# Kernel tuning notes

Measured on AMD Instinct MI355X. Metric: run time of the kernel, lower is better.

The kernel has to match this reference:

```python
import jax, jax.numpy as jnp
import numpy as np

N_NODES = 10000
N_EDGES = 100000
IN_CH = 384
PROJ = 768  # in_channels * projection_factor
N_BLOCKS = 4
OUT_CH = 128
LN_EPS = 1e-5


def _p(key, shape, fan_in):
    return jax.random.normal(key, shape, dtype=jnp.float32) * (1.0 / np.sqrt(fan_in))


def setup_inputs() -> dict:
    key = jax.random.key(0)
    ks = iter(jax.random.split(key, 64))
    x = jax.random.normal(next(ks), (N_NODES, IN_CH), dtype=jnp.float32)
    edge_index = jax.random.randint(next(ks), (2, N_EDGES), 0, N_NODES, dtype=jnp.int64)
    inp = {
        'x': x,
        'edge_index': edge_index,
        'proj_W': _p(next(ks), (PROJ, IN_CH), IN_CH),
        'proj_b': jnp.zeros((PROJ,), jnp.float32),
        'norm_w': jnp.ones((N_BLOCKS, PROJ), jnp.float32),
        'norm_b': jnp.zeros((N_BLOCKS, PROJ), jnp.float32),
        'g1_W': _p(next(ks), (N_BLOCKS, 4 * 192, PROJ), PROJ),
        'g1_as': _p(next(ks), (N_BLOCKS, 4, 192), 192),
        'g1_ad': _p(next(ks), (N_BLOCKS, 4, 192), 192),
        'g1_b': jnp.zeros((N_BLOCKS, 4 * 192), jnp.float32),
        'g2_W': _p(next(ks), (N_BLOCKS, 2 * 96, PROJ), PROJ),
        'g2_as': _p(next(ks), (N_BLOCKS, 2, 96), 96),
        'g2_ad': _p(next(ks), (N_BLOCKS, 2, 96), 96),
        'g2_b': jnp.zeros((N_BLOCKS, 2 * 96), jnp.float32),
        'uni_W': _p(next(ks), (N_BLOCKS, PROJ, 960), 960),
        'uni_b': jnp.zeros((N_BLOCKS, PROJ), jnp.float32),
        'fnorm_w': jnp.ones((PROJ,), jnp.float32),
        'fnorm_b': jnp.zeros((PROJ,), jnp.float32),
        'fg_W': _p(next(ks), (8 * OUT_CH, PROJ), PROJ),
        'fg_as': _p(next(ks), (8, OUT_CH), OUT_CH),
        'fg_ad': _p(next(ks), (8, OUT_CH), OUT_CH),
        'fg_b': jnp.zeros((OUT_CH,), jnp.float32),
    }
    return inp


def layer_norm(x, w, b):
    m = x.mean(-1, keepdims=True)
    v = ((x - m) ** 2).mean(-1, keepdims=True)
    return (x - m) / jnp.sqrt(v + LN_EPS) * w + b


def gat_conv(x, src, dst, W, a_src, a_dst, bias, heads, out_ch, concat):
    # PyG GATConv (eval mode, add_self_loops already applied in src/dst).
    n = x.shape[0]
    h = (x @ W.T).reshape(n, heads, out_ch)          # [N,H,C]
    al_s = jnp.einsum('nhc,hc->nh', h, a_src)        # [N,H]
    al_d = jnp.einsum('nhc,hc->nh', h, a_dst)
    e = jax.nn.leaky_relu(al_s[src] + al_d[dst], 0.2)  # [E,H]
    emax = jax.ops.segment_max(e, dst, num_segments=n)
    ee = jnp.exp(e - emax[dst])
    den = jax.ops.segment_sum(ee, dst, num_segments=n)
    alpha = ee / (den[dst] + 1e-16)                  # softmax over incoming edges
    out = jax.ops.segment_sum(h[src] * alpha[:, :, None], dst, num_segments=n)
    out = out.reshape(n, heads * out_ch) if concat else out.mean(axis=1)
    return out + bias


def reference(x, edge_index, proj_W, proj_b, norm_w, norm_b,
              g1_W, g1_as, g1_ad, g1_b, g2_W, g2_as, g2_ad, g2_b,
              uni_W, uni_b, fnorm_w, fnorm_b, fg_W, fg_as, fg_ad, fg_b):
    n = x.shape[0]
    loop = jnp.arange(n, dtype=edge_index.dtype)
    src = jnp.concatenate([edge_index[0], loop])  # add self loops (PyG default)
    dst = jnp.concatenate([edge_index[1], loop])

    h = jax.nn.elu(x @ proj_W.T + proj_b)
    for i in range(N_BLOCKS):
        res = h
        hn = layer_norm(h, norm_w[i], norm_b[i])
        o1 = gat_conv(hn, src, dst, g1_W[i], g1_as[i], g1_ad[i], g1_b[i], 4, 192, True)
        o2 = gat_conv(hn, src, dst, g2_W[i], g2_as[i], g2_ad[i], g2_b[i], 2, 96, True)
        cat = jax.nn.elu(jnp.concatenate([o1, o2], axis=-1))  # [N,960]
        h = jax.nn.elu(res + cat @ uni_W[i].T + uni_b[i])
    h = layer_norm(h, fnorm_w, fnorm_b)
    return gat_conv(h, src, dst, fg_W, fg_as, fg_ad, fg_b, 8, OUT_CH, False)
```

## Files before the change

### kernel.cpp

```cpp
#include <hip/hip_runtime.h>
#include <math.h>

#define N_NODES 10000
#define N_EDGES 100000
#define E_TOT   (N_EDGES + N_NODES)
#define PROJ    768
#define LN_EPS  1e-5f

typedef __attribute__((ext_vector_type(8))) short bf16x8;
typedef __attribute__((ext_vector_type(4))) short bf16x4;
typedef __attribute__((ext_vector_type(4))) float f32x4;

__device__ __forceinline__ float elu_f(float x){ return x > 0.f ? x : __expf(x) - 1.f; }
__device__ __forceinline__ float bf2f(unsigned short u){ return __uint_as_float(((unsigned int)u) << 16); }
__device__ __forceinline__ unsigned short f2bf(float f){
  unsigned int u = __float_as_uint(f);
  return (unsigned short)((u + 0x7FFFu + ((u >> 16) & 1u)) >> 16);
}

#define GLOAD16(gp, lp) __builtin_amdgcn_global_load_lds((const __attribute__((address_space(1))) void*)(gp), (__attribute__((address_space(3))) void*)(lp), 16, 0, 0)

__global__ void k_count(const int* __restrict__ ei, int* __restrict__ cnt){
  int e = blockIdx.x*blockDim.x + threadIdx.x;
  if (e >= E_TOT) return;
  int dst = (e < N_EDGES) ? ei[N_EDGES + e] : (e - N_EDGES);
  atomicAdd(&cnt[dst], 1);
}

__global__ void k_scan(const int* __restrict__ cnt, int* __restrict__ indptr){
  __shared__ int s[1024];
  __shared__ int s_running;
  int t = threadIdx.x;
  if (t == 0) s_running = 0;
  __syncthreads();
  for (int base = 0; base < N_NODES; base += 1024){
    int v = (base + t < N_NODES) ? cnt[base + t] : 0;
    s[t] = v; __syncthreads();
    for (int off = 1; off < 1024; off <<= 1){
      int add = (t >= off) ? s[t - off] : 0;
      __syncthreads();
      s[t] += add;
      __syncthreads();
    }
    int total = s[1023];
    int run = s_running;
    if (base + t < N_NODES) indptr[base + t] = run + s[t] - v;
    __syncthreads();
    if (t == 0) s_running = run + total;
    __syncthreads();
  }
  if (t == 0) indptr[N_NODES] = s_running;
}

__global__ void k_copy_int(const int* __restrict__ src, int* __restrict__ dst, int n){
  int i = blockIdx.x*blockDim.x + threadIdx.x;
  if (i < n) dst[i] = src[i];
}

__global__ void k_fill(const int* __restrict__ ei, int* __restrict__ pos, int* __restrict__ csr_src){
  int e = blockIdx.x*blockDim.x + threadIdx.x;
  if (e >= E_TOT) return;
  int s, d;
  if (e < N_EDGES){ s = ei[e]; d = ei[N_EDGES + e]; }
  else            { s = d = e - N_EDGES; }
  int p = atomicAdd(&pos[d], 1);
  csr_src[p] = s;
}

__global__ void k_f2bf_arr4(const float4* __restrict__ in, ushort4* __restrict__ out, int n4){
  int i = blockIdx.x*blockDim.x + threadIdx.x;
  if (i < n4){
    float4 v = in[i];
    ushort4 o;
    o.x = f2bf(v.x); o.y = f2bf(v.y); o.z = f2bf(v.z); o.w = f2bf(v.w);
    out[i] = o;
  }
}

__global__ void k_pack_l1l2(const float* __restrict__ g1, const float* __restrict__ g2,
                            unsigned short* __restrict__ dst){
  int i = blockIdx.x*blockDim.x + threadIdx.x;
  if (i >= 737280) return;
  int layer = i / 184320;
  int off4  = i - layer*184320;
  float4 v;
  if (off4 < 147456) v = *((const float4*)(g1 + (size_t)layer*589824) + off4);
  else               v = *((const float4*)(g2 + (size_t)layer*147456) + (off4 - 147456));
  ushort4 o;
  o.x = f2bf(v.x); o.y = f2bf(v.y); o.z = f2bf(v.z); o.w = f2bf(v.w);
  ((ushort4*)(dst + (size_t)layer*737280))[off4] = o;
}

__global__ void k_layernorm_bf(const float* __restrict__ x, const float* __restrict__ w,
                               const float* __restrict__ b, unsigned short* __restrict__ y){
  int n = blockIdx.x;
  int t = threadIdx.x;
  const float* xr = x + (size_t)n*PROJ;
  float v0 = xr[t], v1 = xr[t+256], v2 = xr[t+512];
  float s  = v0+v1+v2;
  float s2 = v0*v0 + v1*v1 + v2*v2;
  #pragma unroll
  for (int off = 32; off; off >>= 1){ s += __shfl_down(s, off); s2 += __shfl_down(s2, off); }
  __shared__ float rs[4], rs2[4];
  __shared__ float s_mean, s_rstd;
  int wid = t >> 6, lane = t & 63;
  if (lane == 0){ rs[wid] = s; rs2[wid] = s2; }
  __syncthreads();
  if (t == 0){
    float S  = rs[0]+rs[1]+rs[2]+rs[3];
    float S2 = rs2[0]+rs2[1]+rs2[2]+rs2[3];
    float m  = S * (1.f/768.f);
    float var = S2 * (1.f/768.f) - m*m;
    s_mean = m; s_rstd = rsqrtf(var + LN_EPS);
  }
  __syncthreads();
  float m = s_mean, r = s_rstd;
  unsigned short* yr = y + (size_t)n*PROJ;
  yr[t]     = f2bf((v0-m)*r*w[t]     + b[t]);
  yr[t+256] = f2bf((v1-m)*r*w[t+256] + b[t+256]);
  yr[t+512] = f2bf((v2-m)*r*w[t+512] + b[t+512]);
}

template<int EPI>
__global__ __launch_bounds__(256)
void k_gemm_mfma(const unsigned short* __restrict__ A, int lda,
                 const unsigned short* __restrict__ W,
                 void* __restrict__ Cv, int ldc,
                 int M, int N, int K,
                 const float* __restrict__ bias,
                 const float* __restrict__ res, int ldres){
  __shared__ unsigned short As[128*32];
  __shared__ unsigned short Bs[128*32];
  const int bm = blockIdx.y*128, bn = blockIdx.x*128;
  const int tid = threadIdx.x;
  const int lane = tid & 63, wid = tid >> 6;
  const int wm = wid >> 1, wn = wid & 1;

  const int rowA0 = tid >> 2;
  const int c8 = (tid & 3) << 3;

  f32x4 acc[4][4];
  #pragma unroll
  for (int i=0;i<4;i++)
    #pragma unroll
    for (int j=0;j<4;j++) acc[i][j] = (f32x4){0.f,0.f,0.f,0.f};

  const size_t amr0 = (size_t)min(bm + rowA0,      M-1) * lda;
  const size_t amr1 = (size_t)min(bm + rowA0 + 64, M-1) * lda;
  const size_t wnr0 = (size_t)min(bn + rowA0,      N-1) * K;
  const size_t wnr1 = (size_t)min(bn + rowA0 + 64, N-1) * K;

  unsigned short* ldsA0 = &As[(wid*64)*8];
  unsigned short* ldsA1 = &As[(256 + wid*64)*8];
  unsigned short* ldsB0 = &Bs[(wid*64)*8];
  unsigned short* ldsB1 = &Bs[(256 + wid*64)*8];

  for (int k0 = 0; k0 < K; k0 += 32){
    __syncthreads();
    GLOAD16(A + amr0 + k0 + c8, ldsA0);
    GLOAD16(A + amr1 + k0 + c8, ldsA1);
    GLOAD16(W + wnr0 + k0 + c8, ldsB0);
    GLOAD16(W + wnr1 + k0 + c8, ldsB1);
    __syncthreads();

    bf16x8 af[4], bfr[4];
    const int kb8 = (lane >> 4) * 8;
    #pragma unroll
    for (int mi=0; mi<4; mi++){
      int r = wm*64 + mi*16 + (lane & 15);
      af[mi] = *(const bf16x8*)&As[r*32 + kb8];
    }
    #pragma unroll
    for (int ni=0; ni<4; ni++){
      int r = wn*64 + ni*16 + (lane & 15);
      bfr[ni] = *(const bf16x8*)&Bs[r*32 + kb8];
    }
    #pragma unroll
    for (int mi=0; mi<4; mi++)
      #pragma unroll
      for (int ni=0; ni<4; ni++)
        acc[mi][ni] = __builtin_amdgcn_mfma_f32_16x16x32_bf16(af[mi], bfr[ni], acc[mi][ni], 0,0,0);
  }

  const int mrow0 = bm + wm*64 + ((lane>>4)<<2);
  const int ncol0 = bn + wn*64 + (lane & 15);
  #pragma unroll
  for (int mi=0; mi<4; mi++){
    #pragma unroll
    for (int r=0; r<4; r++){
      int m = mrow0 + mi*16 + r;
      if (m >= M) continue;
      #pragma unroll
      for (int ni=0; ni<4; ni++){
        int n = ncol0 + ni*16;
        if (n >= N) continue;
        float v = acc[mi][ni][r];
        if (EPI == 0){
          ((unsigned short*)Cv)[(size_t)m*ldc + n] = f2bf(v);
        } else if (EPI == 1){
          ((float*)Cv)[(size_t)m*ldc + n] = elu_f(v + bias[n]);
        } else {
          ((float*)Cv)[(size_t)m*ldc + n] = elu_f(v + bias[n] + res[(size_t)m*ldres + n]);
        }
      }
    }
  }
}

template<int H, int C>
__global__ void k_attn_coef(const unsigned short* __restrict__ hlin, int ldh,
                            const float* __restrict__ a_src,
                            const float* __restrict__ a_dst,
                            float* __restrict__ als, float* __restrict__ ald){
  constexpr int CH = C/4;
  int n = blockIdx.x;
  int wid = threadIdx.x >> 6, lane = threadIdx.x & 63;
  float ss = 0.f, sd = 0.f;
  if (lane < CH){
    bf16x4 hv = *(const bf16x4*)(hlin + (size_t)n*ldh + wid*C + lane*4);
    float4 as_ = *(const float4*)&a_src[wid*C + lane*4];
    float4 ad_ = *(const float4*)&a_dst[wid*C + lane*4];
    float h0 = bf2f((unsigned short)hv.x), h1 = bf2f((unsigned short)hv.y);
    float h2 = bf2f((unsigned short)hv.z), h3 = bf2f((unsigned short)hv.w);
    ss = h0*as_.x + h1*as_.y + h2*as_.z + h3*as_.w;
    sd = h0*ad_.x + h1*ad_.y + h2*ad_.z + h3*ad_.w;
  }
  #pragma unroll
  for (int off = 32; off; off >>= 1){ ss += __shfl_down(ss, off); sd += __shfl_down(sd, off); }
  if (lane == 0){ als[n*H + wid] = ss; ald[n*H + wid] = sd; }
}

template<int H, int C, bool CONCAT, bool DO_ELU>
__global__ __launch_bounds__(256)
void k_attn_agg(const unsigned short* __restrict__ hlin, int ldh,
                const float* __restrict__ als, const float* __restrict__ ald,
                const int* __restrict__ indptr, const int* __restrict__ csr_src,
                const float* __restrict__ bias,
                void* __restrict__ outv, int ldo, int col0){
  constexpr int TOT = H*C;
  constexpr int CHUNKS = TOT/4;
  constexpr int CPL = (CHUNKS + 63)/64;
  int n = blockIdx.x;
  int tid = threadIdx.x;
  int wv = tid >> 6, lane = tid & 63;
  int beg = indptr[n], end = indptr[n+1];

  __shared__ float s_m[H], s_dinv[H], s_ald[H];
  __shared__ float s_red[4][TOT];

  for (int h = wv; h < H; h += 4){
    float aldv = ald[n*H + h];
    float m = -1e30f, d = 0.f;
    for (int e = beg + lane; e < end; e += 64){
      int s = csr_src[e];
      float v = als[s*H + h] + aldv;
      v = v > 0.f ? v : 0.2f*v;
      if (v > m){ d *= __expf(m - v); m = v; }
      d += __expf(v - m);
    }
    #pragma unroll
    for (int off = 1; off < 64; off <<= 1){
      float mo = __shfl_xor(m, off);
      float dd = __shfl_xor(d, off);
      float mn = fmaxf(m, mo);
      d = d*__expf(m - mn) + dd*__expf(mo - mn);
      m = mn;
    }
    if (lane == 0){ s_m[h] = m; s_dinv[h] = 1.f/(d + 1e-16f); s_ald[h] = aldv; }
  }
  __syncthreads();

  int hof[CPL];
  #pragma unroll
  for (int p = 0; p < CPL; p++) hof[p] = ((lane + p*64)*4)/C;

  f32x4 acc[CPL];
  #pragma unroll
  for (int p = 0; p < CPL; p++) acc[p] = (f32x4){0.f,0.f,0.f,0.f};

  for (int e = beg + wv; e < end; e += 4){
    int s = csr_src[e];
    float al = 0.f;
    if (lane < H){
      float v = als[s*H + lane] + s_ald[lane];
      v = v > 0.f ? v : 0.2f*v;
      al = __expf(v - s_m[lane]) * s_dinv[lane];
    }
    float aph[CPL];
    #pragma unroll
    for (int p = 0; p < CPL; p++) aph[p] = __shfl(al, hof[p]);
    const bf16x4* hr = (const bf16x4*)(hlin + (size_t)s*ldh);
    #pragma unroll
    for (int p = 0; p < CPL; p++){
      int ch = lane + p*64;
      if (CHUNKS % 64 == 0 || ch < CHUNKS){
        bf16x4 hv = hr[ch];
        acc[p].x += bf2f((unsigned short)hv.x)*aph[p];
        acc[p].y += bf2f((unsigned short)hv.y)*aph[p];
        acc[p].z += bf2f((unsigned short)hv.z)*aph[p];
        acc[p].w += bf2f((unsigned short)hv.w)*aph[p];
      }
    }
  }

  #pragma unroll
  for (int p = 0; p < CPL; p++){
    int ch = lane + p*64;
    if (CHUNKS % 64 == 0 || ch < CHUNKS)
      *(f32x4*)&s_red[wv][ch*4] = acc[p];
  }
  __syncthreads();

  if (CONCAT){
    unsigned short* out = (unsigned short*)outv;
    constexpr int QS = (TOT + 255)/256;
    #pragma unroll
    for (int q = 0; q < QS; q++){
      int idx = tid + q*256;
      if (TOT % 256 == 0 || idx < TOT){
        float v = s_red[0][idx] + s_red[1][idx] + s_red[2][idx] + s_red[3][idx] + bias[idx];
        if (DO_ELU) v = elu_f(v);
        out[(size_t)n*ldo + col0 + idx] = f2bf(v);
      }
    }
  } else {
    float* out = (float*)outv;
    if (tid < C){
      float v = 0.f;
      #pragma unroll
      for (int h = 0; h < H; h++){
        int idx = h*C + tid;
        v += s_red[0][idx] + s_red[1][idx] + s_red[2][idx] + s_red[3][idx];
      }
      out[(size_t)n*ldo + tid] = v*(1.f/(float)H) + bias[tid];
    }
  }
}

extern "C" void kernel_launch(void* const* d_in, const int* in_sizes, int n_in,
                              void* d_out, int out_size, void* d_ws, size_t ws_size,
                              hipStream_t stream){
  const float* x      = (const float*)d_in[0];
  const int*   ei     = (const int*)  d_in[1];
  const float* proj_W = (const float*)d_in[2];
  const float* proj_b = (const float*)d_in[3];
  const float* norm_w = (const float*)d_in[4];
  const float* norm_b = (const float*)d_in[5];
  const float* g1_W   = (const float*)d_in[6];
  const float* g1_as  = (const float*)d_in[7];
  const float* g1_ad  = (const float*)d_in[8];
  const float* g1_b   = (const float*)d_in[9];
  const float* g2_W   = (const float*)d_in[10];
  const float* g2_as  = (const float*)d_in[11];
  const float* g2_ad  = (const float*)d_in[12];
  const float* g2_b   = (const float*)d_in[13];
  const float* uni_W  = (const float*)d_in[14];
  const float* uni_b  = (const float*)d_in[15];
  const float* fnorm_w= (const float*)d_in[16];
  const float* fnorm_b= (const float*)d_in[17];
  const float* fg_W   = (const float*)d_in[18];
  const float* fg_as  = (const float*)d_in[19];
  const float* fg_ad  = (const float*)d_in[20];
  const float* fg_b   = (const float*)d_in[21];

  float* w = (float*)d_ws;
  float* h    = w; w += 7680000;
  float* h2   = w; w += 7680000;
  unsigned short* linbuf = (unsigned short*)w; w += 5120000;
  unsigned short* hnb  = (unsigned short*)w; w += 3840000;
  unsigned short* catb = (unsigned short*)w; w += 4800000;
  unsigned short* wb   = (unsigned short*)w; w += 3489792;
  float* als  = w; w += 80000;
  float* ald  = w; w += 80000;
  float* als2 = w; w += 80000;
  float* ald2 = w; w += 80000;
  int* iw = (int*)w;
  int* cnt     = iw; iw += 10016;
  int* indptr  = iw; iw += 10016;
  int* pos     = iw; iw += 10016;
  int* csr_src = iw; iw += 110016;

  unsigned short* wb_proj = wb;
  unsigned short* wb_l12  = wb_proj + 294912;
  unsigned short* wb_uni  = wb_l12 + 2949120;
  unsigned short* wb_fg   = wb_uni + 2949120;

  hipMemsetAsync(cnt, 0, N_NODES*sizeof(int), stream);
  k_count<<<(E_TOT+255)/256, 256, 0, stream>>>(ei, cnt);
  k_scan<<<1, 1024, 0, stream>>>(cnt, indptr);
  k_copy_int<<<(N_NODES+255)/256, 256, 0, stream>>>(indptr, pos, N_NODES);
  k_fill<<<(E_TOT+255)/256, 256, 0, stream>>>(ei, pos, csr_src);

  k_f2bf_arr4<<<(960000+255)/256, 256, 0, stream>>>((const float4*)x, (ushort4*)hnb, 960000);
  k_f2bf_arr4<<<(73728+255)/256,  256, 0, stream>>>((const float4*)proj_W, (ushort4*)wb_proj, 73728);
  k_pack_l1l2<<<(737280+255)/256, 256, 0, stream>>>(g1_W, g2_W, wb_l12);
  k_f2bf_arr4<<<(737280+255)/256, 256, 0, stream>>>((const float4*)uni_W, (ushort4*)wb_uni, 737280);
  k_f2bf_arr4<<<(196608+255)/256, 256, 0, stream>>>((const float4*)fg_W, (ushort4*)wb_fg, 196608);

  dim3 blk(256);
  const int GY = (N_NODES + 127) / 128;

  k_gemm_mfma<1><<<dim3(6, GY), blk, 0, stream>>>(hnb, 384, wb_proj, h, 768, N_NODES, 768, 384, proj_b, nullptr, 0);

  float* cur = h;
  float* oth = h2;
  for (int i = 0; i < 4; i++){
    k_layernorm_bf<<<N_NODES, 256, 0, stream>>>(cur, norm_w + i*768, norm_b + i*768, hnb);
    k_gemm_mfma<0><<<dim3(8, GY), blk, 0, stream>>>(hnb, 768, wb_l12 + (size_t)i*737280, linbuf, 960, N_NODES, 960, 768, nullptr, nullptr, 0);
    k_attn_coef<4,192><<<N_NODES, 256, 0, stream>>>(linbuf, 960, g1_as + i*768, g1_ad + i*768, als, ald);
    k_attn_agg<4,192,true,true><<<N_NODES, 256, 0, stream>>>(linbuf, 960, als, ald, indptr, csr_src, g1_b + i*768, catb, 960, 0);
    k_attn_coef<2,96><<<N_NODES, 128, 0, stream>>>(linbuf + 768, 960, g2_as + i*192, g2_ad + i*192, als2, ald2);
    k_attn_agg<2,96,true,true><<<N_NODES, 256, 0, stream>>>(linbuf + 768, 960, als2, ald2, indptr, csr_src, g2_b + i*192, catb, 960, 768);
    k_gemm_mfma<2><<<dim3(6, GY), blk, 0, stream>>>(catb, 960, wb_uni + (size_t)i*737280, oth, 768, N_NODES, 768, 960, uni_b + i*768, cur, 768);
    float* t = cur; cur = oth; oth = t;
  }

  k_layernorm_bf<<<N_NODES, 256, 0, stream>>>(cur, fnorm_w, fnorm_b, hnb);
  k_gemm_mfma<0><<<dim3(8, GY), blk, 0, stream>>>(hnb, 768, wb_fg, linbuf, 1024, N_NODES, 1024, 768, nullptr, nullptr, 0);
  k_attn_coef<8,128><<<N_NODES, 512, 0, stream>>>(linbuf, 1024, fg_as, fg_ad, als, ald);
  k_attn_agg<8,128,false,false><<<N_NODES, 256, 0, stream>>>(linbuf, 1024, als, ald, indptr, csr_src, fg_b, d_out, 128, 0);
}
```

Measured before the change: 835.9 us.

## Double-buffer GEMM LDS tiles with BK=64, XOR swizzle, and XCD-aware block mapping

The MFMA GEMM now loads K-tiles of 64 into two LDS buffers, prefetching the next tile with global_load_lds while computing on the current one. This removes the second barrier per iteration. LDS columns are XOR-swizzled to avoid bank conflicts, and the launch is flattened to a 1D grid remapped so consecutive tiles land on the same XCD for L2 reuse. Launch bounds now request 2 waves per SIMD. The cost is 64KB of LDS per block, which limits occupancy, and the kernel assumes K is a multiple of 64 (384, 768 and 960 all are).

New measurement: 789.6 us. -5.5%, faster.

```diff
diff --git a/kernel.cpp b/kernel.cpp
--- a/kernel.cpp
+++ b/kernel.cpp
@@ -122,22 +122,35 @@
 }
 
 template<int EPI>
-__global__ __launch_bounds__(256)
+__global__ __launch_bounds__(256, 2)
 void k_gemm_mfma(const unsigned short* __restrict__ A, int lda,
                  const unsigned short* __restrict__ W,
                  void* __restrict__ Cv, int ldc,
                  int M, int N, int K,
                  const float* __restrict__ bias,
-                 const float* __restrict__ res, int ldres){
-  __shared__ unsigned short As[128*32];
-  __shared__ unsigned short Bs[128*32];
-  const int bm = blockIdx.y*128, bn = blockIdx.x*128;
+                 const float* __restrict__ res, int ldres, int NBN){
+  __shared__ unsigned short As[2][128*64];
+  __shared__ unsigned short Bs[2][128*64];
   const int tid = threadIdx.x;
   const int lane = tid & 63, wid = tid >> 6;
   const int wm = wid >> 1, wn = wid & 1;
 
-  const int rowA0 = tid >> 2;
-  const int c8 = (tid & 3) << 3;
+  const int nwg = gridDim.x;
+  const int q = nwg >> 3, r = nwg & 7;
+  const int xcd = blockIdx.x & 7, o = blockIdx.x >> 3;
+  const int swz = (xcd < r ? xcd*(q+1) : r*(q+1) + (xcd - r)*q) + o;
+  const int bm = (swz / NBN) * 128;
+  const int bn = (swz % NBN) * 128;
+
+  const int srow = tid >> 3;
+  const int sc16 = (tid & 7) ^ (srow & 7);
+  size_t ga[4], gb[4];
+  #pragma unroll
+  for (int p = 0; p < 4; p++){
+    ga[p] = (size_t)min(bm + p*32 + srow, M-1)*lda + sc16*8;
+    gb[p] = (size_t)min(bn + p*32 + srow, N-1)*K   + sc16*8;
+  }
+  const int ldst = tid*8;
 
   f32x4 acc[4][4];
   #pragma unroll
@@ -145,41 +158,43 @@
     #pragma unroll
     for (int j=0;j<4;j++) acc[i][j] = (f32x4){0.f,0.f,0.f,0.f};
 
-  const size_t amr0 = (size_t)min(bm + rowA0,      M-1) * lda;
-  const size_t amr1 = (size_t)min(bm + rowA0 + 64, M-1) * lda;
-  const size_t wnr0 = (size_t)min(bn + rowA0,      N-1) * K;
-  const size_t wnr1 = (size_t)min(bn + rowA0 + 64, N-1) * K;
-
-  unsigned short* ldsA0 = &As[(wid*64)*8];
-  unsigned short* ldsA1 = &As[(256 + wid*64)*8];
-  unsigned short* ldsB0 = &Bs[(wid*64)*8];
-  unsigned short* ldsB1 = &Bs[(256 + wid*64)*8];
-
-  for (int k0 = 0; k0 < K; k0 += 32){
+  const int rA = wm*64 + (lane & 15);
+  const int rB = wn*64 + (lane & 15);
+
+  const int NT = K >> 6;
+  int cur = 0;
+  #pragma unroll
+  for (int p = 0; p < 4; p++){
+    GLOAD16(A + ga[p], &As[0][p*2048 + ldst]);
+    GLOAD16(W + gb[p], &Bs[0][p*2048 + ldst]);
+  }
+  for (int t = 0; t < NT; ++t){
     __syncthreads();
-    GLOAD16(A + amr0 + k0 + c8, ldsA0);
-    GLOAD16(A + amr1 + k0 + c8, ldsA1);
-    GLOAD16(W + wnr0 + k0 + c8, ldsB0);
-    GLOAD16(W + wnr1 + k0 + c8, ldsB1);
-    __syncthreads();
-
-    bf16x8 af[4], bfr[4];
-    const int kb8 = (lane >> 4) * 8;
-    #pragma unroll
-    for (int mi=0; mi<4; mi++){
-      int r = wm*64 + mi*16 + (lane & 15);
-      af[mi] = *(const bf16x8*)&As[r*32 + kb8];
-    }
-    #pragma unroll
-    for (int ni=0; ni<4; ni++){
-      int r = wn*64 + ni*16 + (lane & 15);
-      bfr[ni] = *(const bf16x8*)&Bs[r*32 + kb8];
-    }
-    #pragma unroll
-    for (int mi=0; mi<4; mi++)
-      #pragma unroll
-      for (int ni=0; ni<4; ni++)
-        acc[mi][ni] = __builtin_amdgcn_mfma_f32_16x16x32_bf16(af[mi], bfr[ni], acc[mi][ni], 0,0,0);
+    if (t + 1 < NT){
+      const int k0 = (t+1) << 6;
+      #pragma unroll
+      for (int p = 0; p < 4; p++){
+        GLOAD16(A + ga[p] + k0, &As[cur^1][p*2048 + ldst]);
+        GLOAD16(W + gb[p] + k0, &Bs[cur^1][p*2048 + ldst]);
+      }
+    }
+    #pragma unroll
+    for (int kk = 0; kk < 2; kk++){
+      bf16x8 af[4], bfr[4];
+      const int cA = (((kk<<2) | (lane>>4)) ^ (lane&7)) * 8;
+      #pragma unroll
+      for (int mi = 0; mi < 4; mi++)
+        af[mi] = *(const bf16x8*)&As[cur][(rA + mi*16)*64 + cA];
+      #pragma unroll
+      for (int ni = 0; ni < 4; ni++)
+        bfr[ni] = *(const bf16x8*)&Bs[cur][(rB + ni*16)*64 + cA];
+      #pragma unroll
+      for (int mi = 0; mi < 4; mi++)
+        #pragma unroll
+        for (int ni = 0; ni < 4; ni++)
+          acc[mi][ni] = __builtin_amdgcn_mfma_f32_16x16x32_bf16(af[mi], bfr[ni], acc[mi][ni], 0,0,0);
+    }
+    cur ^= 1;
   }
 
   const int mrow0 = bm + wm*64 + ((lane>>4)<<2);
@@ -187,14 +202,14 @@
   #pragma unroll
   for (int mi=0; mi<4; mi++){
     #pragma unroll
-    for (int r=0; r<4; r++){
-      int m = mrow0 + mi*16 + r;
+    for (int rr=0; rr<4; rr++){
+      int m = mrow0 + mi*16 + rr;
       if (m >= M) continue;
       #pragma unroll
       for (int ni=0; ni<4; ni++){
         int n = ncol0 + ni*16;
         if (n >= N) continue;
-        float v = acc[mi][ni][r];
+        float v = acc[mi][ni][rr];
         if (EPI == 0){
           ((unsigned short*)Cv)[(size_t)m*ldc + n] = f2bf(v);
         } else if (EPI == 1){
@@ -315,8 +330,8 @@
     unsigned short* out = (unsigned short*)outv;
     constexpr int QS = (TOT + 255)/256;
     #pragma unroll
-    for (int q = 0; q < QS; q++){
-      int idx = tid + q*256;
+    for (int qq = 0; qq < QS; qq++){
+      int idx = tid + qq*256;
       if (TOT % 256 == 0 || idx < TOT){
         float v = s_red[0][idx] + s_red[1][idx] + s_red[2][idx] + s_red[3][idx] + bias[idx];
         if (DO_ELU) v = elu_f(v);
@@ -398,25 +413,25 @@
   k_f2bf_arr4<<<(196608+255)/256, 256, 0, stream>>>((const float4*)fg_W, (ushort4*)wb_fg, 196608);
 
   dim3 blk(256);
-  const int GY = (N_NODES + 127) / 128;
-
-  k_gemm_mfma<1><<<dim3(6, GY), blk, 0, stream>>>(hnb, 384, wb_proj, h, 768, N_NODES, 768, 384, proj_b, nullptr, 0);
+  const int GM = (N_NODES + 127) / 128;
+
+  k_gemm_mfma<1><<<dim3(6*GM), blk, 0, stream>>>(hnb, 384, wb_proj, h, 768, N_NODES, 768, 384, proj_b, nullptr, 0, 6);
 
   float* cur = h;
   float* oth = h2;
   for (int i = 0; i < 4; i++){
     k_layernorm_bf<<<N_NODES, 256, 0, stream>>>(cur, norm_w + i*768, norm_b + i*768, hnb);
-    k_gemm_mfma<0><<<dim3(8, GY), blk, 0, stream>>>(hnb, 768, wb_l12 + (size_t)i*737280, linbuf, 960, N_NODES, 960, 768, nullptr, nullptr, 0);
+    k_gemm_mfma<0><<<dim3(8*GM), blk, 0, stream>>>(hnb, 768, wb_l12 + (size_t)i*737280, linbuf, 960, N_NODES, 960, 768, nullptr, nullptr, 0, 8);
     k_attn_coef<4,192><<<N_NODES, 256, 0, stream>>>(linbuf, 960, g1_as + i*768, g1_ad + i*768, als, ald);
     k_attn_agg<4,192,true,true><<<N_NODES, 256, 0, stream>>>(linbuf, 960, als, ald, indptr, csr_src, g1_b + i*768, catb, 960, 0);
     k_attn_coef<2,96><<<N_NODES, 128, 0, stream>>>(linbuf + 768, 960, g2_as + i*192, g2_ad + i*192, als2, ald2);
     k_attn_agg<2,96,true,true><<<N_NODES, 256, 0, stream>>>(linbuf + 768, 960, als2, ald2, indptr, csr_src, g2_b + i*192, catb, 960, 768);
-    k_gemm_mfma<2><<<dim3(6, GY), blk, 0, stream>>>(catb, 960, wb_uni + (size_t)i*737280, oth, 768, N_NODES, 768, 960, uni_b + i*768, cur, 768);
+    k_gemm_mfma<2><<<dim3(6*GM), blk, 0, stream>>>(catb, 960, wb_uni + (size_t)i*737280, oth, 768, N_NODES, 768, 960, uni_b + i*768, cur, 768, 6);
     float* t = cur; cur = oth; oth = t;
   }
 
   k_layernorm_bf<<<N_NODES, 256, 0, stream>>>(cur, fnorm_w, fnorm_b, hnb);
-  k_gemm_mfma<0><<<dim3(8, GY), blk, 0, stream>>>(hnb, 768, wb_fg, linbuf, 1024, N_NODES, 1024, 768, nullptr, nullptr, 0);
+  k_gemm_mfma<0><<<dim3(8*GM), blk, 0, stream>>>(hnb, 768, wb_fg, linbuf, 1024, N_NODES, 1024, 768, nullptr, nullptr, 0, 8);
   k_attn_coef<8,128><<<N_NODES, 512, 0, stream>>>(linbuf, 1024, fg_as, fg_ad, als, ald);
   k_attn_agg<8,128,false,false><<<N_NODES, 256, 0, stream>>>(linbuf, 1024, als, ald, indptr, csr_src, fg_b, d_out, 128, 0);
 }
```
